# Optimization experiments

Hardware: AMD Instinct MI355X
Metric: run time of the kernel (lower is better)

The kernel has to match this reference:

```python
import jax, jax.numpy as jnp
import numpy as np

NUM_HEADS = 12


def setup_inputs() -> dict:
    key = jax.random.key(0)
    k0, k1, k2 = jax.random.split(key, 3)
    B, S, D = 2, 2048, 1536
    scale = 1.0 / np.sqrt(D)
    return {
        "hidden_states": jax.random.normal(k0, (B, S, D), dtype=jnp.float32),
        "W_fc": jax.random.normal(k1, (D, D), dtype=jnp.float32) * scale,
        "b_fc": jnp.zeros((D,), dtype=jnp.float32),
        "W_proj": jax.random.normal(k2, (D, D), dtype=jnp.float32) * scale,
        "b_proj": jnp.zeros((D,), dtype=jnp.float32),
    }


def reference(hidden_states, W_fc, b_fc, W_proj, b_proj):
    B, S, D = hidden_states.shape
    H = NUM_HEADS
    hd = D // H
    # value_states: [B, H, S, hd] (key_states == value_states in the original)
    v = (hidden_states @ W_fc.T + b_fc).reshape(B, S, H, hd).transpose(0, 2, 1, 3)
    # Uniform-weight causal sliding-window attention, window_h = 2^(h+1)-1.
    i = jnp.arange(S)[:, None]          # query pos
    j = jnp.arange(S)[None, :]          # key pos
    w = (2 ** jnp.arange(1, H + 1, dtype=jnp.int32) - 1)[:, None, None]  # [H,1,1]
    mask = (j <= i) & (j >= i - w + 1)                                    # [H,S,S]
    valid_len = jnp.minimum(i + 1, w).astype(v.dtype)                     # [H,S,1]
    attn = jnp.where(mask, 1.0 / valid_len, 0.0)                          # [H,S,S]
    # [H,S,S] x [B,H,S,hd] -> [B,S,H,hd] -> [B,S,D]
    out = jnp.einsum("hqk,bhkd->bqhd", attn, v).reshape(B, S, D)
    attn_weights = jnp.broadcast_to(attn[None], (B, H, S, S))
    return out @ W_proj.T + b_proj, attn_weights
```

## Files before the change

kernel.cpp:

```cpp
#include <hip/hip_runtime.h>
#include <hip/hip_bf16.h>

#define S_LEN   2048
#define DMODEL  1536
#define NBATCH  2
#define NHEADS  12
#define MROWS   (NBATCH * S_LEN)
#define NCHUNK  64
#define CHUNK   32

typedef unsigned short u16;
typedef __attribute__((ext_vector_type(8))) short bf16x8;
typedef __attribute__((ext_vector_type(4))) float f32x4;

__device__ __forceinline__ u16 f2bf(float x) {
  unsigned u = __float_as_uint(x);
  u += 0x7fffu + ((u >> 16) & 1u);
  return (u16)(u >> 16);
}
__device__ __forceinline__ float bf2f(u16 x) {
  return __uint_as_float(((unsigned)x) << 16);
}

#define N4_HID  1572864
#define N4_W    589824
__global__ void cvt_all(const float4* __restrict__ h, const float4* __restrict__ wf,
                        const float4* __restrict__ wp, ushort4* __restrict__ ho,
                        ushort4* __restrict__ wfo, ushort4* __restrict__ wpo) {
  int t = blockIdx.x * blockDim.x + threadIdx.x;
  const float4* src;
  ushort4* dst;
  int idx;
  if (t < N4_HID)            { src = h;  dst = ho;  idx = t; }
  else if (t < N4_HID + N4_W){ src = wf; dst = wfo; idx = t - N4_HID; }
  else                       { src = wp; dst = wpo; idx = t - N4_HID - N4_W; }
  float4 f = src[idx];
  ushort4 o;
  o.x = f2bf(f.x); o.y = f2bf(f.y); o.z = f2bf(f.z); o.w = f2bf(f.w);
  dst[idx] = o;
}

__device__ __forceinline__ void gld_lds16(u16* lds, const u16* g) {
  __builtin_amdgcn_global_load_lds(
      (const __attribute__((address_space(1))) unsigned int*)g,
      (__attribute__((address_space(3))) unsigned int*)lds, 16, 0, 0);
}

template <bool WITH_CSUM, typename CT>
__global__ __launch_bounds__(256)
void gemm_bt_bias(const u16* __restrict__ A, const u16* __restrict__ B,
                  const float* __restrict__ bias, CT* __restrict__ C,
                  float* __restrict__ cs, int Ndim, int Kdim) {
  __shared__ __align__(16) u16 As[128 * 32];
  __shared__ __align__(16) u16 Bs[128 * 32];
  __shared__ float colpart[4][128];

  const int tid  = threadIdx.x;
  const int wave = tid >> 6;
  const int lane = tid & 63;
  const int l15  = lane & 15;
  const int quad = lane >> 4;
  const int bm = blockIdx.y * 128;
  const int bn = blockIdx.x * 128;
  const int wm = (wave >> 1) * 64;
  const int wn = (wave & 1) * 64;

  f32x4 acc[4][4] = {};

  const int srow = wave * 32 + (lane >> 2);
  const int skk  = (lane & 3) * 8;
  const u16* gA = A + (size_t)(bm + srow) * Kdim + skk;
  const u16* gB = B + (size_t)(bn + srow) * Kdim + skk;
  u16* lA = &As[(wave * 32) * 32];
  u16* lB = &Bs[(wave * 32) * 32];
  const size_t rstep16 = (size_t)16 * Kdim;

  for (int k0 = 0; k0 < Kdim; k0 += 32) {
    gld_lds16(lA,           gA + k0);
    gld_lds16(lA + 16 * 32, gA + k0 + rstep16);
    gld_lds16(lB,           gB + k0);
    gld_lds16(lB + 16 * 32, gB + k0 + rstep16);
    __syncthreads();

    bf16x8 af[4], bfr[4];
#pragma unroll
    for (int i = 0; i < 4; ++i)
      af[i] = *(const bf16x8*)&As[(wm + i * 16 + l15) * 32 + quad * 8];
#pragma unroll
    for (int j = 0; j < 4; ++j)
      bfr[j] = *(const bf16x8*)&Bs[(wn + j * 16 + l15) * 32 + quad * 8];
#pragma unroll
    for (int i = 0; i < 4; ++i)
#pragma unroll
      for (int j = 0; j < 4; ++j)
        acc[i][j] = __builtin_amdgcn_mfma_f32_16x16x32_bf16(af[i], bfr[j], acc[i][j], 0, 0, 0);
    __syncthreads();
  }

  const int r0 = quad * 4;
#pragma unroll
  for (int j = 0; j < 4; ++j) {
    const int col = bn + wn + j * 16 + l15;
    const float bj = bias[col];
    float sA = 0.f, sB = 0.f;
#pragma unroll
    for (int i = 0; i < 4; ++i) {
      const int row = bm + wm + i * 16 + r0;
#pragma unroll
      for (int r = 0; r < 4; ++r) {
        float cv = acc[i][j][r] + bj;
        if constexpr (sizeof(CT) == 2)
          C[(size_t)(row + r) * Ndim + col] = (CT)f2bf(cv);
        else
          C[(size_t)(row + r) * Ndim + col] = (CT)cv;
        if (WITH_CSUM) { if (i < 2) sA += cv; else sB += cv; }
      }
    }
    if (WITH_CSUM) {
      sA += __shfl_xor(sA, 16); sA += __shfl_xor(sA, 32);
      sB += __shfl_xor(sB, 16); sB += __shfl_xor(sB, 32);
      if (quad == 0) {
        colpart[(wm >> 5) | 0][wn + j * 16 + l15] = sA;
        colpart[(wm >> 5) | 1][wn + j * 16 + l15] = sB;
      }
    }
  }
  if (WITH_CSUM) {
    __syncthreads();
    if (tid < 128) {
      const int b  = bm >> 11;
      const int c0 = (bm & 2047) >> 5;
#pragma unroll
      for (int g = 0; g < 4; ++g)
        cs[((size_t)b * NCHUNK + c0 + g) * DMODEL + bn + tid] = colpart[g][tid];
    }
  }
}

__global__ void winavg_fused(const u16* __restrict__ v, const float* __restrict__ cs,
                             u16* __restrict__ A2) {
  int t = blockIdx.x * blockDim.x + threadIdx.x;
  int d = t % DMODEL;
  int c = (t / DMODEL) % NCHUNK;
  int b = t / (DMODEL * NCHUNK);
  const int h = d >> 7;
  const int w = (2 << h) - 1;
  const u16* vb = v + (size_t)b * S_LEN * DMODEL + d;
  const float* csb = cs + (size_t)b * NCHUNK * DMODEL + d;

  const int i0 = c * CHUNK;
  float lead = 0.f;
  for (int cc = 0; cc < c; ++cc) lead += csb[(size_t)cc * DMODEL];

  float trail = 0.f;
  const int tstart = i0 - w;
  if (tstart > 0) {
    const int tc = tstart >> 5;
    for (int cc = 0; cc < tc; ++cc) trail += csb[(size_t)cc * DMODEL];
#pragma unroll 4
    for (int r = tc * CHUNK; r < tstart; ++r) trail += bf2f(vb[(size_t)r * DMODEL]);
  }

  u16* out = A2 + ((size_t)(b * S_LEN + i0)) * DMODEL + d;
#pragma unroll 4
  for (int r = 0; r < CHUNK; ++r) {
    const int i = i0 + r;
    lead += bf2f(vb[(size_t)i * DMODEL]);
    float o;
    if (i < w) {
      o = lead / (float)(i + 1);
    } else {
      trail += bf2f(vb[(size_t)(i - w) * DMODEL]);
      o = (lead - trail) / (float)w;
    }
    out[(size_t)r * DMODEL] = f2bf(o);
  }
}

__global__ void attn_weights_kernel(float4* __restrict__ out4) {
  int t = blockIdx.x * blockDim.x + threadIdx.x;
  int j0 = (t & 511) << 2;
  int i  = (t >> 9) & (S_LEN - 1);
  int bh = t >> 20;
  int h  = bh >= NHEADS ? bh - NHEADS : bh;
  int w  = (2 << h) - 1;
  int len = min(i + 1, w);
  float inv = 1.0f / (float)len;
  int lo = i - w + 1;
  float4 r;
  r.x = (j0     <= i && j0     >= lo) ? inv : 0.f;
  r.y = (j0 + 1 <= i && j0 + 1 >= lo) ? inv : 0.f;
  r.z = (j0 + 2 <= i && j0 + 2 >= lo) ? inv : 0.f;
  r.w = (j0 + 3 <= i && j0 + 3 >= lo) ? inv : 0.f;
  out4[t] = r;
}

extern "C" void kernel_launch(void* const* d_in, const int* in_sizes, int n_in,
                              void* d_out, int out_size, void* d_ws, size_t ws_size,
                              hipStream_t stream) {
  const float* hidden = (const float*)d_in[0];
  const float* W_fc   = (const float*)d_in[1];
  const float* b_fc   = (const float*)d_in[2];
  const float* W_proj = (const float*)d_in[3];
  const float* b_proj = (const float*)d_in[4];
  float* outp = (float*)d_out;

  char* ws = (char*)d_ws;
  u16*   A16   = (u16*)(ws);
  u16*   Wfc16 = (u16*)(ws + 12582912);
  u16*   Wpj16 = (u16*)(ws + 17301504);
  u16*   v16   = (u16*)(ws + 22020096);
  float* csums = (float*)(ws + 34603008);

  cvt_all<<<10752, 256, 0, stream>>>((const float4*)hidden, (const float4*)W_fc,
                                     (const float4*)W_proj, (ushort4*)A16,
                                     (ushort4*)Wfc16, (ushort4*)Wpj16);

  gemm_bt_bias<true, u16><<<dim3(DMODEL / 128, MROWS / 128), 256, 0, stream>>>(
      A16, Wfc16, b_fc, v16, csums, DMODEL, DMODEL);

  winavg_fused<<<(NBATCH * NCHUNK * DMODEL) / 256, 256, 0, stream>>>(v16, csums, A16);

  gemm_bt_bias<false, float><<<dim3(DMODEL / 128, MROWS / 128), 256, 0, stream>>>(
      A16, Wpj16, b_proj, outp, nullptr, DMODEL, DMODEL);

  attn_weights_kernel<<<(NBATCH * NHEADS * S_LEN * S_LEN / 4) / 256, 256, 0, stream>>>(
      (float4*)(outp + (size_t)MROWS * DMODEL));
}
```

Before: 567.9 us.

## Split window average into chunk-prefix pass and finer 8-row strips; nontemporal attn stores

The sliding-window averaging is split into two kernels. The first computes exclusive prefix sums of the per-chunk column sums. The second runs one thread per 8-row strip instead of per 32-row chunk, giving four times more threads, and starts its lead and trail sums from the precomputed prefixes plus up to 31 row reads. The attention-weights writer now uses nontemporal stores to avoid polluting caches with its large write-only output. This costs an extra launch and more redundant v reads per row.

```diff
diff --git a/kernel.cpp b/kernel.cpp
--- a/kernel.cpp
+++ b/kernel.cpp
@@ -137,34 +137,48 @@
   }
 }
 
-__global__ void winavg_fused(const u16* __restrict__ v, const float* __restrict__ cs,
-                             u16* __restrict__ A2) {
+__global__ void chunk_prefix(const float* __restrict__ cs, float* __restrict__ E) {
   int t = blockIdx.x * blockDim.x + threadIdx.x;
   int d = t % DMODEL;
   int c = (t / DMODEL) % NCHUNK;
   int b = t / (DMODEL * NCHUNK);
+  const float* p = cs + (size_t)b * NCHUNK * DMODEL + d;
+  float s = 0.f;
+  for (int cc = 0; cc < c; ++cc) s += p[(size_t)cc * DMODEL];
+  E[t] = s;
+}
+
+__global__ void winavg_strip(const u16* __restrict__ v, const float* __restrict__ E,
+                             u16* __restrict__ A2) {
+  int t = blockIdx.x * blockDim.x + threadIdx.x;
+  int d = t % DMODEL;
+  int s = (t / DMODEL) & 255;
+  int b = t / (DMODEL * 256);
   const int h = d >> 7;
   const int w = (2 << h) - 1;
-  const u16* vb = v + (size_t)b * S_LEN * DMODEL + d;
-  const float* csb = cs + (size_t)b * NCHUNK * DMODEL + d;
-
-  const int i0 = c * CHUNK;
-  float lead = 0.f;
-  for (int cc = 0; cc < c; ++cc) lead += csb[(size_t)cc * DMODEL];
+  const u16* vb  = v + (size_t)b * S_LEN * DMODEL + d;
+  const float* Eb = E + (size_t)b * NCHUNK * DMODEL + d;
+
+  const int i0 = s * 8;
+  float lead = Eb[(size_t)(i0 >> 5) * DMODEL];
+  for (int r = i0 & ~31; r < i0; ++r)
+    lead += bf2f(vb[(size_t)r * DMODEL]);
 
   float trail = 0.f;
-  const int tstart = i0 - w;
-  if (tstart > 0) {
-    const int tc = tstart >> 5;
-    for (int cc = 0; cc < tc; ++cc) trail += csb[(size_t)cc * DMODEL];
-#pragma unroll 4
-    for (int r = tc * CHUNK; r < tstart; ++r) trail += bf2f(vb[(size_t)r * DMODEL]);
+  if (i0 + 7 >= w) {
+    const int jf = max(i0, w) - w;
+    if (jf > 0) {
+      const int ct = (jf - 1) >> 5;
+      trail = Eb[(size_t)ct * DMODEL];
+      for (int r = ct * 32; r < jf; ++r)
+        trail += bf2f(vb[(size_t)r * DMODEL]);
+    }
   }
 
   u16* out = A2 + ((size_t)(b * S_LEN + i0)) * DMODEL + d;
-#pragma unroll 4
-  for (int r = 0; r < CHUNK; ++r) {
-    const int i = i0 + r;
+#pragma unroll
+  for (int rr = 0; rr < 8; ++rr) {
+    const int i = i0 + rr;
     lead += bf2f(vb[(size_t)i * DMODEL]);
     float o;
     if (i < w) {
@@ -173,11 +187,11 @@
       trail += bf2f(vb[(size_t)(i - w) * DMODEL]);
       o = (lead - trail) / (float)w;
     }
-    out[(size_t)r * DMODEL] = f2bf(o);
-  }
-}
-
-__global__ void attn_weights_kernel(float4* __restrict__ out4) {
+    out[(size_t)rr * DMODEL] = f2bf(o);
+  }
+}
+
+__global__ void attn_weights_kernel(f32x4* __restrict__ out4) {
   int t = blockIdx.x * blockDim.x + threadIdx.x;
   int j0 = (t & 511) << 2;
   int i  = (t >> 9) & (S_LEN - 1);
@@ -187,12 +201,12 @@
   int len = min(i + 1, w);
   float inv = 1.0f / (float)len;
   int lo = i - w + 1;
-  float4 r;
+  f32x4 r;
   r.x = (j0     <= i && j0     >= lo) ? inv : 0.f;
   r.y = (j0 + 1 <= i && j0 + 1 >= lo) ? inv : 0.f;
   r.z = (j0 + 2 <= i && j0 + 2 >= lo) ? inv : 0.f;
   r.w = (j0 + 3 <= i && j0 + 3 >= lo) ? inv : 0.f;
-  out4[t] = r;
+  __builtin_nontemporal_store(r, &out4[t]);
 }
 
 extern "C" void kernel_launch(void* const* d_in, const int* in_sizes, int n_in,
@@ -211,6 +225,7 @@
   u16*   Wpj16 = (u16*)(ws + 17301504);
   u16*   v16   = (u16*)(ws + 22020096);
   float* csums = (float*)(ws + 34603008);
+  float* Epre  = (float*)(ws + 35389440);
 
   cvt_all<<<10752, 256, 0, stream>>>((const float4*)hidden, (const float4*)W_fc,
                                      (const float4*)W_proj, (ushort4*)A16,
@@ -219,11 +234,13 @@
   gemm_bt_bias<true, u16><<<dim3(DMODEL / 128, MROWS / 128), 256, 0, stream>>>(
       A16, Wfc16, b_fc, v16, csums, DMODEL, DMODEL);
 
-  winavg_fused<<<(NBATCH * NCHUNK * DMODEL) / 256, 256, 0, stream>>>(v16, csums, A16);
+  chunk_prefix<<<(NBATCH * NCHUNK * DMODEL) / 256, 256, 0, stream>>>(csums, Epre);
+
+  winavg_strip<<<(NBATCH * (S_LEN / 8) * DMODEL) / 256, 256, 0, stream>>>(v16, Epre, A16);
 
   gemm_bt_bias<false, float><<<dim3(DMODEL / 128, MROWS / 128), 256, 0, stream>>>(
       A16, Wpj16, b_proj, outp, nullptr, DMODEL, DMODEL);
 
   attn_weights_kernel<<<(NBATCH * NHEADS * S_LEN * S_LEN / 4) / 256, 256, 0, stream>>>(
-      (float4*)(outp + (size_t)MROWS * DMODEL));
-}
+      (f32x4*)(outp + (size_t)MROWS * DMODEL));
+}
```

Measured after the change: 574.6 us. Within noise of the previous version (+1.2%).
